# Optimization experiments

Hardware: AMD Instinct MI355X
Metric: run time of the kernel (lower is better)

The kernel has to match this reference:

```python
import jax, jax.numpy as jnp
import numpy as np

BS, C, H, W = 8, 64, 128, 128
KS = 3
SCALE = 2


def _pose_map(src_h, src_w, scale):
    # Vectorized version of positionKPN.pose_map (bilinear source coords).
    dst_h, dst_w = int(np.floor(src_h * scale)), int(np.floor(src_w * scale))
    scale_x, scale_y = float(src_w) / dst_w, float(src_h) / dst_h
    src_x = (np.arange(dst_w) + 0.5) * scale_x - 0.5
    src_y = (np.arange(dst_h) + 0.5) * scale_y - 0.5
    x0, y0 = np.floor(src_x), np.floor(src_y)
    inter_x = np.broadcast_to((x0 + 1).astype(np.int32)[None, :], (dst_h, dst_w))
    inter_y = np.broadcast_to((y0 + 1).astype(np.int32)[:, None], (dst_h, dst_w))
    fx = np.broadcast_to((src_x - x0).astype(np.float32)[None, :], (dst_h, dst_w))
    fy = np.broadcast_to((src_y - y0).astype(np.float32)[:, None], (dst_h, dst_w))
    pose = np.stack([fx, fy], axis=0).astype(np.float32)  # [2, dst_h, dst_w]
    return pose, np.ascontiguousarray(inter_y), np.ascontiguousarray(inter_x)


def setup_inputs() -> dict:
    key = jax.random.key(0)
    ks = jax.random.split(key, 8)
    pose, inter_y, inter_x = _pose_map(H, W, SCALE)
    s = 0.05
    return {
        "x": jax.random.normal(ks[0], (BS, C, H, W), dtype=jnp.float32),
        "scale": SCALE,
        "poseMap": jnp.asarray(pose),
        "interMapY": jnp.asarray(inter_y),
        "interMapX": jnp.asarray(inter_x),
        "W1": jax.random.normal(ks[1], (128, 2), dtype=jnp.float32) * s,
        "b1": jnp.zeros((128,), dtype=jnp.float32),
        "W2": jax.random.normal(ks[2], (256, 128), dtype=jnp.float32) * s,
        "b2": jnp.zeros((256,), dtype=jnp.float32),
        "W3": jax.random.normal(ks[3], (C * KS * KS, 256), dtype=jnp.float32) * s,
        "b3": jnp.zeros((C * KS * KS,), dtype=jnp.float32),
    }


def reference(x, scale, poseMap, interMapY, interMapX, W1, b1, W2, b2, W3, b3):
    bs, cs, h, w = x.shape
    ho, wo = interMapY.shape
    k2 = KS * KS
    # 1x1-conv MLP on position map -> per-pixel dynamic kernels.
    h1 = jax.nn.relu(jnp.einsum('oc,chw->ohw', W1, poseMap) + b1[:, None, None])
    h2 = jax.nn.relu(jnp.einsum('oc,chw->ohw', W2, h1) + b2[:, None, None])
    wgt = jnp.einsum('oc,chw->ohw', W3, h2) + b3[:, None, None]  # [cs*k2, ho, wo]
    wgt = wgt.reshape(cs, k2, ho, wo)
    # 3x3 patches gathered at source-grid centers interMap in [0, h] x [0, w]
    # (patch center y needs rows y-1..y+1 of x -> pad 1 before, 2 after).
    pad = KS // 2
    xp = jnp.pad(x, ((0, 0), (0, 0), (pad, pad + 1), (pad, pad + 1)))
    ky, kx = jnp.meshgrid(jnp.arange(KS), jnp.arange(KS), indexing='ij')
    Y = interMapY[None, :, :] + ky.reshape(k2, 1, 1)  # [k2, ho, wo]
    X = interMapX[None, :, :] + kx.reshape(k2, 1, 1)
    taps = xp[:, :, Y, X]  # [bs, cs, k2, ho, wo]
    out = jnp.einsum('bckyx,ckyx->bcyx', taps, wgt)  # per-pixel dynamic depthwise conv
    return out
```

## Files before the change

### kernel.cpp

```cpp
#include <hip/hip_runtime.h>

#define H_IN   128
#define W_IN   128
#define H_OUT  256
#define W_OUT  256
#define C_CH   64
#define B_SZ   8

typedef float vfloat4 __attribute__((ext_vector_type(4)));

__device__ __forceinline__ float rfl(float v) {
    return __uint_as_float(__builtin_amdgcn_readfirstlane(__float_as_uint(v)));
}

__global__ __launch_bounds__(576) void kpn_mlp(
    const float* __restrict__ pose,
    const float* __restrict__ W1,
    const float* __restrict__ b1,
    const float* __restrict__ W2,
    const float* __restrict__ b2,
    const float* __restrict__ W3,
    const float* __restrict__ b3,
    float* __restrict__ wgt4)
{
    __shared__ float h1[128];
    __shared__ float h2[256];

    const int p  = blockIdx.x;
    const int py = p >> 1, px = p & 1;
    const int t  = threadIdx.x;

    const float fx = pose[0 * H_OUT * W_OUT + py * W_OUT + px];
    const float fy = pose[1 * H_OUT * W_OUT + py * W_OUT + px];

    if (t < 128) {
        float a = W1[t * 2 + 0] * fx + W1[t * 2 + 1] * fy + b1[t];
        h1[t] = a > 0.f ? a : 0.f;
    }
    __syncthreads();

    if (t < 256) {
        float acc = b2[t];
        const float4* w = (const float4*)(W2 + t * 128);
        #pragma unroll 8
        for (int k = 0; k < 32; ++k) {
            float4 wv = w[k];
            acc += wv.x * h1[4 * k + 0] + wv.y * h1[4 * k + 1]
                 + wv.z * h1[4 * k + 2] + wv.w * h1[4 * k + 3];
        }
        h2[t] = acc > 0.f ? acc : 0.f;
    }
    __syncthreads();

    {
        float acc = b3[t];
        const float4* w = (const float4*)(W3 + t * 256);
        #pragma unroll 16
        for (int k = 0; k < 64; ++k) {
            float4 wv = w[k];
            acc += wv.x * h2[4 * k + 0] + wv.y * h2[4 * k + 1]
                 + wv.z * h2[4 * k + 2] + wv.w * h2[4 * k + 3];
        }
        const int c = t / 9, k = t - c * 9;
        wgt4[c * 48 + p * 12 + k] = acc;
    }
}

__global__ __launch_bounds__(256, 4) void kpn_apply(
    const float* __restrict__ x,
    const float* __restrict__ wgt4,
    float* __restrict__ out)
{
    const int l    = threadIdx.x;
    const int wgid = blockIdx.x * 4 + threadIdx.y;
    const int bc   = wgid >> 3;
    const int i0   = (wgid & 7) * 16;
    const int c    = bc & 63;

    float wt[4][9];
    const float* wp = wgt4 + c * 48;
    #pragma unroll
    for (int p = 0; p < 4; ++p) {
        float4 a = *(const float4*)(wp + p * 12);
        float4 b = *(const float4*)(wp + p * 12 + 4);
        float  g = wp[p * 12 + 8];
        wt[p][0] = rfl(a.x); wt[p][1] = rfl(a.y); wt[p][2] = rfl(a.z); wt[p][3] = rfl(a.w);
        wt[p][4] = rfl(b.x); wt[p][5] = rfl(b.y); wt[p][6] = rfl(b.z); wt[p][7] = rfl(b.w);
        wt[p][8] = rfl(g);
    }

    const float* xp = x + (size_t)bc * (H_IN * W_IN) + 2 * l;
    const int    R0 = i0 - 1;

    float2 v[8];
    float M[4], Ax[4], Bx[4], Dx[4], Ex[4];

    auto issue = [&](int r) {
        int rr = R0 + r;
        int rc = rr < 0 ? 0 : (rr > H_IN - 1 ? H_IN - 1 : rr);
        v[r & 7] = *(const float2*)(xp + rc * W_IN);
    };
    auto expand = [&](int r) {
        const int rr = R0 + r;
        const bool ok = ((unsigned)rr < (unsigned)H_IN);
        float ax = ok ? v[r & 7].x : 0.f;
        float bx = ok ? v[r & 7].y : 0.f;
        float m = __shfl_up(bx, 1, 64);   if (l == 0)  m = 0.f;
        float d = __shfl_down(ax, 1, 64); if (l == 63) d = 0.f;
        float e = __shfl_down(bx, 1, 64); if (l == 63) e = 0.f;
        const int s = r & 3;
        M[s] = m; Ax[s] = ax; Bx[s] = bx; Dx[s] = d; Ex[s] = e;
    };

    #pragma unroll
    for (int r = 0; r < 8; ++r) issue(r);
    #pragma unroll
    for (int r = 0; r < 3; ++r) expand(r);

    float* op = out + ((size_t)bc * H_OUT + 2 * (size_t)i0) * W_OUT + 4 * l;

    #pragma unroll
    for (int q = 0; q < 16; ++q) {
        if (q + 8 < 19) issue(q + 8);
        expand(q + 3);

        float ox0 = 0.f, ox1 = 0.f, ox2 = 0.f, ox3 = 0.f;
        float oy0 = 0.f, oy1 = 0.f, oy2 = 0.f, oy3 = 0.f;
        #pragma unroll
        for (int ky = 0; ky < 3; ++ky) {
            const int su = (q + ky) & 3;
            const int sl = (q + ky + 1) & 3;
            const float w0a = wt[0][3*ky+0], w0b = wt[0][3*ky+1], w0c = wt[0][3*ky+2];
            const float w1a = wt[1][3*ky+0], w1b = wt[1][3*ky+1], w1c = wt[1][3*ky+2];
            const float w2a = wt[2][3*ky+0], w2b = wt[2][3*ky+1], w2c = wt[2][3*ky+2];
            const float w3a = wt[3][3*ky+0], w3b = wt[3][3*ky+1], w3c = wt[3][3*ky+2];
            ox0 += w0a * M[su]  + w0b * Ax[su] + w0c * Bx[su];
            ox1 += w1a * Ax[su] + w1b * Bx[su] + w1c * Dx[su];
            ox2 += w0a * Ax[su] + w0b * Bx[su] + w0c * Dx[su];
            ox3 += w1a * Bx[su] + w1b * Dx[su] + w1c * Ex[su];
            oy0 += w2a * M[sl]  + w2b * Ax[sl] + w2c * Bx[sl];
            oy1 += w3a * Ax[sl] + w3b * Bx[sl] + w3c * Dx[sl];
            oy2 += w2a * Ax[sl] + w2b * Bx[sl] + w2c * Dx[sl];
            oy3 += w3a * Bx[sl] + w3b * Dx[sl] + w3c * Ex[sl];
        }
        vfloat4 r0 = { ox0, ox1, ox2, ox3 };
        vfloat4 r1 = { oy0, oy1, oy2, oy3 };
        __builtin_nontemporal_store(r0, (vfloat4*)op);
        __builtin_nontemporal_store(r1, (vfloat4*)(op + W_OUT));
        op += 2 * W_OUT;
    }
}

extern "C" void kernel_launch(void* const* d_in, const int* in_sizes, int n_in,
                              void* d_out, int out_size, void* d_ws, size_t ws_size,
                              hipStream_t stream) {
    const float* x      = (const float*)d_in[0];
    const float* pose   = (const float*)d_in[2];
    const float* W1     = (const float*)d_in[5];
    const float* b1     = (const float*)d_in[6];
    const float* W2     = (const float*)d_in[7];
    const float* b2     = (const float*)d_in[8];
    const float* W3     = (const float*)d_in[9];
    const float* b3     = (const float*)d_in[10];
    float*       out    = (float*)d_out;
    float*       wgt4   = (float*)d_ws;

    kpn_mlp<<<dim3(4), dim3(576), 0, stream>>>(pose, W1, b1, W2, b2, W3, b3, wgt4);
    kpn_apply<<<dim3(1024), dim3(64, 4), 0, stream>>>(x, wgt4, out);
}
```

Baseline: 53.19 us.

## Remap apply kernel to interleaved row chunks with next-chunk prefetch

Each wave now processes eight scattered single-row chunks, strided across the grid with an XCD-style block swizzle, instead of one contiguous 16-row strip. Loads for the next chunk are issued before computing the current one, and the grid doubles to 2048 blocks. The aim is more even spread of memory traffic across dies and channels plus more parallelism. The cost is that vertically adjacent input rows are reloaded about four times per output row pair, where the old sliding window read each once, and per-chunk weights are reloaded too.

```diff
diff --git a/kernel.cpp b/kernel.cpp
--- a/kernel.cpp
+++ b/kernel.cpp
@@ -66,70 +66,78 @@
     }
 }
 
-__global__ __launch_bounds__(256, 4) void kpn_apply(
+__global__ __launch_bounds__(256) void kpn_apply(
     const float* __restrict__ x,
     const float* __restrict__ wgt4,
     float* __restrict__ out)
 {
-    const int l    = threadIdx.x;
-    const int wgid = blockIdx.x * 4 + threadIdx.y;
-    const int bc   = wgid >> 3;
-    const int i0   = (wgid & 7) * 16;
-    const int c    = bc & 63;
+    const int l   = threadIdx.x;
+    const int wv  = threadIdx.y;
+    const int bid = blockIdx.x;
+    const int sb  = (bid & 7) * 256 + (bid >> 3);
 
-    float wt[4][9];
-    const float* wp = wgt4 + c * 48;
-    #pragma unroll
-    for (int p = 0; p < 4; ++p) {
-        float4 a = *(const float4*)(wp + p * 12);
-        float4 b = *(const float4*)(wp + p * 12 + 4);
-        float  g = wp[p * 12 + 8];
-        wt[p][0] = rfl(a.x); wt[p][1] = rfl(a.y); wt[p][2] = rfl(a.z); wt[p][3] = rfl(a.w);
-        wt[p][4] = rfl(b.x); wt[p][5] = rfl(b.y); wt[p][6] = rfl(b.z); wt[p][7] = rfl(b.w);
-        wt[p][8] = rfl(g);
-    }
+    const int NCHUNK = 16384;
 
-    const float* xp = x + (size_t)bc * (H_IN * W_IN) + 2 * l;
-    const int    R0 = i0 - 1;
-
-    float2 v[8];
-    float M[4], Ax[4], Bx[4], Dx[4], Ex[4];
-
-    auto issue = [&](int r) {
-        int rr = R0 + r;
-        int rc = rr < 0 ? 0 : (rr > H_IN - 1 ? H_IN - 1 : rr);
-        v[r & 7] = *(const float2*)(xp + rc * W_IN);
-    };
-    auto expand = [&](int r) {
-        const int rr = R0 + r;
-        const bool ok = ((unsigned)rr < (unsigned)H_IN);
-        float ax = ok ? v[r & 7].x : 0.f;
-        float bx = ok ? v[r & 7].y : 0.f;
-        float m = __shfl_up(bx, 1, 64);   if (l == 0)  m = 0.f;
-        float d = __shfl_down(ax, 1, 64); if (l == 63) d = 0.f;
-        float e = __shfl_down(bx, 1, 64); if (l == 63) e = 0.f;
-        const int s = r & 3;
-        M[s] = m; Ax[s] = ax; Bx[s] = bx; Dx[s] = d; Ex[s] = e;
+    auto geom = [&](int it, int& bc, int& i) {
+        int ch = it * 2048 + sb;
+        bc = ch >> 5;
+        i  = (ch & 31) * 4 + wv;
     };
 
-    #pragma unroll
-    for (int r = 0; r < 8; ++r) issue(r);
-    #pragma unroll
-    for (int r = 0; r < 3; ++r) expand(r);
+    auto issue = [&](int bc, int i, float2* dst) {
+        const float* xp = x + (size_t)bc * (H_IN * W_IN) + 2 * l;
+        #pragma unroll
+        for (int r = 0; r < 4; ++r) {
+            int rr = i - 1 + r;
+            int rc = rr < 0 ? 0 : (rr > H_IN - 1 ? H_IN - 1 : rr);
+            dst[r] = *(const float2*)(xp + rc * W_IN);
+        }
+    };
 
-    float* op = out + ((size_t)bc * H_OUT + 2 * (size_t)i0) * W_OUT + 4 * l;
+    int bcC, iC, bcN, iN;
+    float2 vC[4], vN[4];
+
+    geom(0, bcC, iC);
+    issue(bcC, iC, vC);
 
     #pragma unroll
-    for (int q = 0; q < 16; ++q) {
-        if (q + 8 < 19) issue(q + 8);
-        expand(q + 3);
+    for (int it = 0; it < 8; ++it) {
+        const int itn = (it < 7) ? it + 1 : 7;
+        geom(itn, bcN, iN);
+        issue(bcN, iN, vN);
+
+        const int c = bcC & 63;
+        float wt[4][9];
+        const float* wp = wgt4 + c * 48;
+        #pragma unroll
+        for (int p = 0; p < 4; ++p) {
+            float4 a = *(const float4*)(wp + p * 12);
+            float4 b = *(const float4*)(wp + p * 12 + 4);
+            float  g = wp[p * 12 + 8];
+            wt[p][0] = rfl(a.x); wt[p][1] = rfl(a.y); wt[p][2] = rfl(a.z); wt[p][3] = rfl(a.w);
+            wt[p][4] = rfl(b.x); wt[p][5] = rfl(b.y); wt[p][6] = rfl(b.z); wt[p][7] = rfl(b.w);
+            wt[p][8] = rfl(g);
+        }
+
+        float M[4], Ax[4], Bx[4], Dx[4], Ex[4];
+        #pragma unroll
+        for (int r = 0; r < 4; ++r) {
+            const int rr = iC - 1 + r;
+            const bool ok = ((unsigned)rr < (unsigned)H_IN);
+            float ax = ok ? vC[r].x : 0.f;
+            float bx = ok ? vC[r].y : 0.f;
+            float m = __shfl_up(bx, 1, 64);   if (l == 0)  m = 0.f;
+            float d = __shfl_down(ax, 1, 64); if (l == 63) d = 0.f;
+            float e = __shfl_down(bx, 1, 64); if (l == 63) e = 0.f;
+            M[r] = m; Ax[r] = ax; Bx[r] = bx; Dx[r] = d; Ex[r] = e;
+        }
 
         float ox0 = 0.f, ox1 = 0.f, ox2 = 0.f, ox3 = 0.f;
         float oy0 = 0.f, oy1 = 0.f, oy2 = 0.f, oy3 = 0.f;
         #pragma unroll
         for (int ky = 0; ky < 3; ++ky) {
-            const int su = (q + ky) & 3;
-            const int sl = (q + ky + 1) & 3;
+            const int su = ky;
+            const int sl = ky + 1;
             const float w0a = wt[0][3*ky+0], w0b = wt[0][3*ky+1], w0c = wt[0][3*ky+2];
             const float w1a = wt[1][3*ky+0], w1b = wt[1][3*ky+1], w1c = wt[1][3*ky+2];
             const float w2a = wt[2][3*ky+0], w2b = wt[2][3*ky+1], w2c = wt[2][3*ky+2];
@@ -143,12 +151,17 @@
             oy2 += w2a * Ax[sl] + w2b * Bx[sl] + w2c * Dx[sl];
             oy3 += w3a * Bx[sl] + w3b * Dx[sl] + w3c * Ex[sl];
         }
+        float* op = out + ((size_t)bcC * H_OUT + 2 * (size_t)iC) * W_OUT + 4 * l;
         vfloat4 r0 = { ox0, ox1, ox2, ox3 };
         vfloat4 r1 = { oy0, oy1, oy2, oy3 };
         __builtin_nontemporal_store(r0, (vfloat4*)op);
         __builtin_nontemporal_store(r1, (vfloat4*)(op + W_OUT));
-        op += 2 * W_OUT;
+
+        bcC = bcN; iC = iN;
+        #pragma unroll
+        for (int r = 0; r < 4; ++r) vC[r] = vN[r];
     }
+    (void)NCHUNK;
 }
 
 extern "C" void kernel_launch(void* const* d_in, const int* in_sizes, int n_in,
@@ -166,5 +179,5 @@
     float*       wgt4   = (float*)d_ws;
 
     kpn_mlp<<<dim3(4), dim3(576), 0, stream>>>(pose, W1, b1, W2, b2, W3, b3, wgt4);
-    kpn_apply<<<dim3(1024), dim3(64, 4), 0, stream>>>(x, wgt4, out);
+    kpn_apply<<<dim3(2048), dim3(64, 4), 0, stream>>>(x, wgt4, out);
 }
```

New measurement: 53.70 us. No clear change (+1.0%).

## Stage whole input planes in LDS and process two planes per block

Applied to the files above, without the earlier changes.

The apply kernel now copies each full 128x128 input plane into a 64 KB shared-memory tile and reads rows from LDS instead of prefetching overlapping global rows per wave. Each block handles two (batch, channel) planes in sequence, with 256 blocks of 4 waves each covering 32 output row-pairs per wave. This removes redundant halo reads and register-staged prefetching. The cost is large LDS use per block, which limits occupancy, and fewer blocks (256) with a serial copy, sync and compute phase per plane that does not overlap load and compute.

```diff
diff --git a/kernel.cpp b/kernel.cpp
--- a/kernel.cpp
+++ b/kernel.cpp
@@ -66,88 +66,95 @@
     }
 }
 
-__global__ __launch_bounds__(256, 4) void kpn_apply(
+__global__ __launch_bounds__(256) void kpn_apply(
     const float* __restrict__ x,
     const float* __restrict__ wgt4,
     float* __restrict__ out)
 {
-    const int l    = threadIdx.x;
-    const int wgid = blockIdx.x * 4 + threadIdx.y;
-    const int bc   = wgid >> 3;
-    const int i0   = (wgid & 7) * 16;
-    const int c    = bc & 63;
+    __shared__ float2 lds[H_IN][W_IN / 2];
 
-    float wt[4][9];
-    const float* wp = wgt4 + c * 48;
-    #pragma unroll
-    for (int p = 0; p < 4; ++p) {
-        float4 a = *(const float4*)(wp + p * 12);
-        float4 b = *(const float4*)(wp + p * 12 + 4);
-        float  g = wp[p * 12 + 8];
-        wt[p][0] = rfl(a.x); wt[p][1] = rfl(a.y); wt[p][2] = rfl(a.z); wt[p][3] = rfl(a.w);
-        wt[p][4] = rfl(b.x); wt[p][5] = rfl(b.y); wt[p][6] = rfl(b.z); wt[p][7] = rfl(b.w);
-        wt[p][8] = rfl(g);
-    }
+    const int t  = threadIdx.x;
+    const int l  = t & 63;
+    const int wv = t >> 6;
 
-    const float* xp = x + (size_t)bc * (H_IN * W_IN) + 2 * l;
-    const int    R0 = i0 - 1;
+    #pragma unroll 1
+    for (int half = 0; half < 2; ++half) {
+        const int bc = blockIdx.x + half * 256;
+        const int c  = bc & 63;
 
-    float2 v[8];
-    float M[4], Ax[4], Bx[4], Dx[4], Ex[4];
+        if (half) __syncthreads();
+        {
+            const float4* src = (const float4*)(x + (size_t)bc * (H_IN * W_IN));
+            float4* dst = (float4*)&lds[0][0];
+            #pragma unroll
+            for (int k = 0; k < 16; ++k)
+                dst[t + k * 256] = src[t + k * 256];
+        }
 
-    auto issue = [&](int r) {
-        int rr = R0 + r;
-        int rc = rr < 0 ? 0 : (rr > H_IN - 1 ? H_IN - 1 : rr);
-        v[r & 7] = *(const float2*)(xp + rc * W_IN);
-    };
-    auto expand = [&](int r) {
-        const int rr = R0 + r;
-        const bool ok = ((unsigned)rr < (unsigned)H_IN);
-        float ax = ok ? v[r & 7].x : 0.f;
-        float bx = ok ? v[r & 7].y : 0.f;
-        float m = __shfl_up(bx, 1, 64);   if (l == 0)  m = 0.f;
-        float d = __shfl_down(ax, 1, 64); if (l == 63) d = 0.f;
-        float e = __shfl_down(bx, 1, 64); if (l == 63) e = 0.f;
-        const int s = r & 3;
-        M[s] = m; Ax[s] = ax; Bx[s] = bx; Dx[s] = d; Ex[s] = e;
-    };
+        float wt[4][9];
+        {
+            const float* wp = wgt4 + c * 48;
+            #pragma unroll
+            for (int p = 0; p < 4; ++p) {
+                float4 a = *(const float4*)(wp + p * 12);
+                float4 b = *(const float4*)(wp + p * 12 + 4);
+                float  g = wp[p * 12 + 8];
+                wt[p][0] = rfl(a.x); wt[p][1] = rfl(a.y); wt[p][2] = rfl(a.z); wt[p][3] = rfl(a.w);
+                wt[p][4] = rfl(b.x); wt[p][5] = rfl(b.y); wt[p][6] = rfl(b.z); wt[p][7] = rfl(b.w);
+                wt[p][8] = rfl(g);
+            }
+        }
+        __syncthreads();
 
-    #pragma unroll
-    for (int r = 0; r < 8; ++r) issue(r);
-    #pragma unroll
-    for (int r = 0; r < 3; ++r) expand(r);
+        const int i0 = 32 * wv;
 
-    float* op = out + ((size_t)bc * H_OUT + 2 * (size_t)i0) * W_OUT + 4 * l;
+        float M[4], Ax[4], Bx[4], Dx[4], Ex[4];
+        auto expand = [&](int r) {
+            const bool ok = ((unsigned)r < (unsigned)H_IN);
+            float ax = 0.f, bx = 0.f;
+            if (ok) { float2 v = lds[r][l]; ax = v.x; bx = v.y; }
+            float m = __shfl_up(bx, 1, 64);   if (l == 0)  m = 0.f;
+            float d = __shfl_down(ax, 1, 64); if (l == 63) d = 0.f;
+            float e = __shfl_down(bx, 1, 64); if (l == 63) e = 0.f;
+            const int s = r & 3;
+            M[s] = m; Ax[s] = ax; Bx[s] = bx; Dx[s] = d; Ex[s] = e;
+        };
 
-    #pragma unroll
-    for (int q = 0; q < 16; ++q) {
-        if (q + 8 < 19) issue(q + 8);
-        expand(q + 3);
+        expand(i0 - 1);
+        expand(i0);
+        expand(i0 + 1);
 
-        float ox0 = 0.f, ox1 = 0.f, ox2 = 0.f, ox3 = 0.f;
-        float oy0 = 0.f, oy1 = 0.f, oy2 = 0.f, oy3 = 0.f;
-        #pragma unroll
-        for (int ky = 0; ky < 3; ++ky) {
-            const int su = (q + ky) & 3;
-            const int sl = (q + ky + 1) & 3;
-            const float w0a = wt[0][3*ky+0], w0b = wt[0][3*ky+1], w0c = wt[0][3*ky+2];
-            const float w1a = wt[1][3*ky+0], w1b = wt[1][3*ky+1], w1c = wt[1][3*ky+2];
-            const float w2a = wt[2][3*ky+0], w2b = wt[2][3*ky+1], w2c = wt[2][3*ky+2];
-            const float w3a = wt[3][3*ky+0], w3b = wt[3][3*ky+1], w3c = wt[3][3*ky+2];
-            ox0 += w0a * M[su]  + w0b * Ax[su] + w0c * Bx[su];
-            ox1 += w1a * Ax[su] + w1b * Bx[su] + w1c * Dx[su];
-            ox2 += w0a * Ax[su] + w0b * Bx[su] + w0c * Dx[su];
-            ox3 += w1a * Bx[su] + w1b * Dx[su] + w1c * Ex[su];
-            oy0 += w2a * M[sl]  + w2b * Ax[sl] + w2c * Bx[sl];
-            oy1 += w3a * Ax[sl] + w3b * Bx[sl] + w3c * Dx[sl];
-            oy2 += w2a * Ax[sl] + w2b * Bx[sl] + w2c * Dx[sl];
-            oy3 += w3a * Bx[sl] + w3b * Dx[sl] + w3c * Ex[sl];
+        float* op = out + ((size_t)bc * H_OUT + 2 * (size_t)i0) * W_OUT + 4 * l;
+
+        #pragma unroll 4
+        for (int q = i0; q < i0 + 32; ++q) {
+            expand(q + 2);
+
+            float ox0 = 0.f, ox1 = 0.f, ox2 = 0.f, ox3 = 0.f;
+            float oy0 = 0.f, oy1 = 0.f, oy2 = 0.f, oy3 = 0.f;
+            #pragma unroll
+            for (int ky = 0; ky < 3; ++ky) {
+                const int su = (q - 1 + ky) & 3;
+                const int sl = (q + ky) & 3;
+                const float w0a = wt[0][3*ky+0], w0b = wt[0][3*ky+1], w0c = wt[0][3*ky+2];
+                const float w1a = wt[1][3*ky+0], w1b = wt[1][3*ky+1], w1c = wt[1][3*ky+2];
+                const float w2a = wt[2][3*ky+0], w2b = wt[2][3*ky+1], w2c = wt[2][3*ky+2];
+                const float w3a = wt[3][3*ky+0], w3b = wt[3][3*ky+1], w3c = wt[3][3*ky+2];
+                ox0 += w0a * M[su]  + w0b * Ax[su] + w0c * Bx[su];
+                ox1 += w1a * Ax[su] + w1b * Bx[su] + w1c * Dx[su];
+                ox2 += w0a * Ax[su] + w0b * Bx[su] + w0c * Dx[su];
+                ox3 += w1a * Bx[su] + w1b * Dx[su] + w1c * Ex[su];
+                oy0 += w2a * M[sl]  + w2b * Ax[sl] + w2c * Bx[sl];
+                oy1 += w3a * Ax[sl] + w3b * Bx[sl] + w3c * Dx[sl];
+                oy2 += w2a * Ax[sl] + w2b * Bx[sl] + w2c * Dx[sl];
+                oy3 += w3a * Bx[sl] + w3b * Dx[sl] + w3c * Ex[sl];
+            }
+            vfloat4 r0 = { ox0, ox1, ox2, ox3 };
+            vfloat4 r1 = { oy0, oy1, oy2, oy3 };
+            __builtin_nontemporal_store(r0, (vfloat4*)op);
+            __builtin_nontemporal_store(r1, (vfloat4*)(op + W_OUT));
+            op += 2 * W_OUT;
         }
-        vfloat4 r0 = { ox0, ox1, ox2, ox3 };
-        vfloat4 r1 = { oy0, oy1, oy2, oy3 };
-        __builtin_nontemporal_store(r0, (vfloat4*)op);
-        __builtin_nontemporal_store(r1, (vfloat4*)(op + W_OUT));
-        op += 2 * W_OUT;
     }
 }
 
@@ -166,5 +173,5 @@
     float*       wgt4   = (float*)d_ws;
 
     kpn_mlp<<<dim3(4), dim3(576), 0, stream>>>(pose, W1, b1, W2, b2, W3, b3, wgt4);
-    kpn_apply<<<dim3(1024), dim3(64, 4), 0, stream>>>(x, wgt4, out);
+    kpn_apply<<<dim3(256), dim3(256), 0, stream>>>(x, wgt4, out);
 }
```

Result: slower. 59.47 us (+11.8%).
